# Optimization experiments

Hardware: AMD Instinct MI355X
Metric: run time of the kernel (lower is better)

The kernel has to match this reference:

```python
import jax, jax.numpy as jnp
import numpy as np

H = 1024  # hidden_size
NH = 16   # num_heads
HD = H // NH  # head_dim

def setup_inputs() -> dict:
    key = jax.random.key(0)
    ks = jax.random.split(key, 7)
    s = 1.0 / np.sqrt(H)
    return {
        "hidden": jax.random.normal(ks[0], (2, 2048, H), dtype=jnp.float32),
        "Wq": jax.random.normal(ks[1], (H, H), dtype=jnp.float32) * s,
        "bq": jnp.zeros((H,), dtype=jnp.float32),
        "Wk": jax.random.normal(ks[2], (H, H), dtype=jnp.float32) * s,
        "bk": jnp.zeros((H,), dtype=jnp.float32),
        "Wv": jax.random.normal(ks[3], (H, H), dtype=jnp.float32) * s,
        "bv": jnp.zeros((H,), dtype=jnp.float32),
    }

def _split_heads(x):
    # [B, S, H] -> [B, NH, S, HD]
    b, s, _ = x.shape
    return x.reshape(b, s, NH, HD).transpose(0, 2, 1, 3)

def reference(hidden, Wq, bq, Wk, bk, Wv, bv):
    q = _split_heads(hidden @ Wq.T + bq)
    k = _split_heads(hidden @ Wk.T + bk)
    v = _split_heads(hidden @ Wv.T + bv)
    scores = jnp.einsum("bhqd,bhkd->bhqk", q, k) / jnp.sqrt(jnp.float32(HD))
    probs = jax.nn.softmax(scores, axis=-1)  # dropout is identity in eval
    ctx = jnp.einsum("bhqk,bhkd->bhqd", probs, v)
    b, _, s, _ = ctx.shape
    return ctx.transpose(0, 2, 1, 3).reshape(b, s, NH * HD)
```

## Files before the change

### kernel.cpp

```cpp
#include <hip/hip_runtime.h>


typedef __attribute__((ext_vector_type(8))) short bf16x8;
typedef __attribute__((ext_vector_type(4))) short bf16x4;
typedef __attribute__((ext_vector_type(4))) float f32x4;

#define L2E 1.44269504088896340736f

__device__ __forceinline__ f32x4 mfma16(bf16x4 a, bf16x4 b, f32x4 c) {
#if defined(__AMDGCN__)
  return __builtin_amdgcn_mfma_f32_16x16x16bf16_1k(a, b, c, 0, 0, 0);
#else
  return c;
#endif
}

__device__ __forceinline__ unsigned short f2bf(float x) {
  union { float f; unsigned int u; } a; a.f = x;
  unsigned int r = (a.u + 0x7fffu + ((a.u >> 16) & 1u)) >> 16;
  return (unsigned short)r;
}
__device__ __forceinline__ unsigned int fbits(float x) {
  union { float f; unsigned int u; } a; a.f = x; return a.u;
}

__device__ __forceinline__ bf16x4 pack_bf16x4(float p0, float p1, float p2, float p3) {
#if defined(__AMDGCN__) && __has_builtin(__builtin_amdgcn_cvt_pk_bf16_f32)
  typedef __attribute__((ext_vector_type(2))) __bf16 bf16x2_t;
  union { bf16x2_t h[2]; bf16x4 v; } pk;
  pk.h[0] = __builtin_amdgcn_cvt_pk_bf16_f32(p0, p1);
  pk.h[1] = __builtin_amdgcn_cvt_pk_bf16_f32(p2, p3);
  return pk.v;
#else
  unsigned u0 = fbits(p0) + 0x8000u, u1 = fbits(p1) + 0x8000u;
  unsigned u2 = fbits(p2) + 0x8000u, u3 = fbits(p3) + 0x8000u;
  union { unsigned u[2]; bf16x4 v; } pk;
  pk.u[0] = __builtin_amdgcn_perm(u1, u0, 0x07060302u);
  pk.u[1] = __builtin_amdgcn_perm(u3, u2, 0x07060302u);
  return pk.v;
#endif
}

__device__ __forceinline__ void gl_lds16(const unsigned short* g, unsigned short* l) {
  __builtin_amdgcn_global_load_lds(
      (const __attribute__((address_space(1))) void*)g,
      (__attribute__((address_space(3))) void*)l, 16, 0, 0);
}

__global__ __launch_bounds__(256) void convert_all(
    const float* __restrict__ hidden, const float* __restrict__ Wq,
    const float* __restrict__ Wk, const float* __restrict__ Wv,
    unsigned short* __restrict__ Xb, unsigned short* __restrict__ Wqb,
    unsigned short* __restrict__ Wkb, unsigned short* __restrict__ Wvb) {
  int i = blockIdx.x * 256 + threadIdx.x;
  const float* src; unsigned short* dst; int off;
  if (i < 1048576)      { src = hidden; dst = Xb;  off = i; }
  else if (i < 1310720) { src = Wq;     dst = Wqb; off = i - 1048576; }
  else if (i < 1572864) { src = Wk;     dst = Wkb; off = i - 1310720; }
  else                  { src = Wv;     dst = Wvb; off = i - 1572864; }
  float4 v = ((const float4*)src)[off];
  ushort4 o;
  o.x = f2bf(v.x); o.y = f2bf(v.y); o.z = f2bf(v.z); o.w = f2bf(v.w);
  ((ushort4*)dst)[off] = o;
}

__global__ __launch_bounds__(256) void qkv_gemm(
    const unsigned short* __restrict__ Xb,
    const unsigned short* __restrict__ Wqb, const unsigned short* __restrict__ Wkb,
    const unsigned short* __restrict__ Wvb,
    const float* __restrict__ bq, const float* __restrict__ bk,
    const float* __restrict__ bv,
    unsigned short* __restrict__ Qh, unsigned short* __restrict__ Kh,
    unsigned short* __restrict__ Vh) {
  const int id  = blockIdx.x;
  const int xcd = id & 7;
  const int j   = id >> 3;
  const int tok = xcd * 4 + (j & 3);
  const int k2  = j >> 2;
  const int ft  = k2 & 7;
  const int z   = k2 >> 3;

  const unsigned short* Ap; const unsigned short* Bp;
  const float* bias; unsigned short* Out; int m0, n0;
  if (z == 2) {
    Ap = Wvb; Bp = Xb; bias = bv; Out = Vh;
    m0 = ft * 128; n0 = tok * 128;
  } else {
    Ap = Xb; Bp = (z == 0) ? Wqb : Wkb; bias = (z == 0) ? bq : bk;
    Out = (z == 0) ? Qh : Kh;
    m0 = tok * 128; n0 = ft * 128;
  }
  const float oscale = (z == 0) ? (0.125f * L2E) : 1.0f;

  __shared__ unsigned short As[128 * 64];
  __shared__ unsigned short Bs[128 * 64];

  const int tid  = threadIdx.x;
  const int lane = tid & 63;
  const int w    = tid >> 6;
  const int wm   = w >> 1, wn = w & 1;
  const int quad = lane >> 4;
  const int r    = lane & 15;

  f32x4 acc[4][4];
#pragma unroll
  for (int a = 0; a < 4; a++)
#pragma unroll
    for (int c = 0; c < 4; c++) acc[a][c] = (f32x4){0.f, 0.f, 0.f, 0.f};

  for (int k0 = 0; k0 < 1024; k0 += 64) {
    __syncthreads();
#pragma unroll
    for (int i = 0; i < 4; i++) {
      int t   = w * 4 + i;
      int blk = t * 64 + lane;
      int row = blk >> 3;
      int c   = (blk & 7) ^ (row & 7);
      gl_lds16(Ap + (size_t)(m0 + row) * 1024 + k0 + c * 8, &As[t * 512]);
      gl_lds16(Bp + (size_t)(n0 + row) * 1024 + k0 + c * 8, &Bs[t * 512]);
    }
    __syncthreads();

    bf16x8 af[4][2], bfv[4][2];
#pragma unroll
    for (int mi = 0; mi < 4; mi++)
#pragma unroll
      for (int ks = 0; ks < 2; ks++) {
        int row = wm * 64 + mi * 16 + r;
        int bc  = (ks * 4 + quad) ^ (row & 7);
        af[mi][ks] = *(const bf16x8*)&As[row * 64 + bc * 8];
      }
#pragma unroll
    for (int ni = 0; ni < 4; ni++)
#pragma unroll
      for (int ks = 0; ks < 2; ks++) {
        int row = wn * 64 + ni * 16 + r;
        int bc  = (ks * 4 + quad) ^ (row & 7);
        bfv[ni][ks] = *(const bf16x8*)&Bs[row * 64 + bc * 8];
      }
#pragma unroll
    for (int mi = 0; mi < 4; mi++)
#pragma unroll
      for (int ni = 0; ni < 4; ni++) {
        acc[mi][ni] = __builtin_amdgcn_mfma_f32_16x16x32_bf16(af[mi][0], bfv[ni][0], acc[mi][ni], 0, 0, 0);
        acc[mi][ni] = __builtin_amdgcn_mfma_f32_16x16x32_bf16(af[mi][1], bfv[ni][1], acc[mi][ni], 0, 0, 0);
      }
  }

  if (z == 2) {
#pragma unroll
    for (int mi = 0; mi < 4; mi++)
#pragma unroll
      for (int e = 0; e < 4; e++) {
        int m = m0 + wm * 64 + mi * 16 + quad * 4 + e;
        float bm = bias[m];
#pragma unroll
        for (int ni = 0; ni < 4; ni++) {
          int n = n0 + wn * 64 + ni * 16 + r;
          int bb = n >> 11, s = n & 2047;
          int hh = m >> 6,  d = m & 63;
          float v = acc[mi][ni][e] + bm;
          Out[((size_t)(bb * 16 + hh) * 64 + d) * 2048 + s] = f2bf(v);
        }
      }
  } else {
    float biasv[4];
#pragma unroll
    for (int ni = 0; ni < 4; ni++) biasv[ni] = bias[n0 + wn * 64 + ni * 16 + r];
#pragma unroll
    for (int mi = 0; mi < 4; mi++)
#pragma unroll
      for (int ni = 0; ni < 4; ni++)
#pragma unroll
        for (int e = 0; e < 4; e++) {
          int m = m0 + wm * 64 + mi * 16 + quad * 4 + e;
          int n = n0 + wn * 64 + ni * 16 + r;
          int bb = m >> 11, s = m & 2047;
          int hh = n >> 6,  d = n & 63;
          float v = (acc[mi][ni][e] + biasv[ni]) * oscale;
          Out[((size_t)(bb * 16 + hh) * 2048 + s) * 64 + d] = f2bf(v);
        }
  }
}

__global__ __launch_bounds__(256, 8) void attn(
    const unsigned short* __restrict__ Qh, const unsigned short* __restrict__ Kh,
    const unsigned short* __restrict__ Vh, float* __restrict__ accP,
    float* __restrict__ lP) {
  const int h = blockIdx.y;
  const int b = blockIdx.z >> 1;
  const int half = blockIdx.z & 1;
  const int bh = b * 16 + h;
  const int q0 = blockIdx.x * 64;
  const unsigned short* Qp  = Qh + (size_t)bh * 2048 * 64;
  const unsigned short* Kp  = Kh + (size_t)bh * 2048 * 64;
  const unsigned short* VTp = Vh + (size_t)bh * 64 * 2048;

  __shared__ unsigned short Ks[64 * 64];
  __shared__ unsigned short Vts[64 * 64];

  const int tid  = threadIdx.x;
  const int lane = tid & 63;
  const int w    = tid >> 6;
  const int quad = lane >> 4;
  const int r    = lane & 15;
  const int rm7  = r & 7;

  const unsigned short* qrow = Qp + (size_t)(q0 + w * 16 + r) * 64 + quad * 8;
  bf16x8 aq0 = *(const bf16x8*)(qrow);
  bf16x8 aq1 = *(const bf16x8*)(qrow + 32);

  float lsum = 0.f;
  f32x4 acc[4];
#pragma unroll
  for (int dc = 0; dc < 4; dc++) acc[dc] = (f32x4){0.f, 0.f, 0.f, 0.f};
  const f32x4 zero4 = (f32x4){0.f, 0.f, 0.f, 0.f};

  const int kx0 = quad ^ rm7;
  const int kx1 = (4 + quad) ^ rm7;
  const int qh2 = quad >> 1, ql4 = (quad & 1) * 4;

  const int kvbase = half * 1024;
  for (int kv0 = kvbase; kv0 < kvbase + 1024; kv0 += 64) {
    __syncthreads();
#pragma unroll
    for (int i = 0; i < 2; i++) {
      int blk = i * 256 + tid;
      int row = blk >> 3;
      int cs  = blk & 7;
      gl_lds16(Kp + (size_t)(kv0 + row) * 64 + ((cs ^ (row & 7)) * 8), &Ks[blk * 8]);
      gl_lds16(VTp + (size_t)row * 2048 + kv0 + (((cs + 5 * row) & 7) * 8), &Vts[blk * 8]);
    }
    __syncthreads();

#pragma unroll
    for (int nc = 0; nc < 4; nc++) {
      int krow = nc * 16 + r;
      bf16x8 kf0 = *(const bf16x8*)&Ks[krow * 64 + kx0 * 8];
      bf16x8 kf1 = *(const bf16x8*)&Ks[krow * 64 + kx1 * 8];

      f32x4 t0 = __builtin_amdgcn_mfma_f32_16x16x32_bf16(kf1, aq1, zero4, 0, 0, 0);
      f32x4 sT = __builtin_amdgcn_mfma_f32_16x16x32_bf16(kf0, aq0, t0, 0, 0, 0);

      float p0 = __builtin_exp2f(sT[0]);
      float p1 = __builtin_exp2f(sT[1]);
      float p2 = __builtin_exp2f(sT[2]);
      float p3 = __builtin_exp2f(sT[3]);
      lsum += (p0 + p1) + (p2 + p3);
      bf16x4 ap = pack_bf16x4(p0, p1, p2, p3);

#pragma unroll
      for (int dc = 0; dc < 4; dc++) {
        int vrow = dc * 16 + r;
        int slot = (2 * nc + qh2 + 3 * vrow) & 7;
        bf16x4 vf = *(const bf16x4*)&Vts[vrow * 64 + slot * 8 + ql4];
        acc[dc] = mfma16(ap, vf, acc[dc]);
      }
    }
  }

  lsum += __shfl_xor(lsum, 16, 64);
  lsum += __shfl_xor(lsum, 32, 64);
  if (lane < 16)
    lP[(size_t)half * 65536 + ((size_t)(b * 2048 + q0 + w * 16 + lane)) * 16 + h] = lsum;

  float* accp = accP + (size_t)half * 4194304;
#pragma unroll
  for (int e = 0; e < 4; e++) {
    int s = q0 + w * 16 + quad * 4 + e;
#pragma unroll
    for (int dc = 0; dc < 4; dc++) {
      int d = dc * 16 + r;
      accp[(size_t)(b * 2048 + s) * 1024 + h * 64 + d] = acc[dc][e];
    }
  }
}

__global__ __launch_bounds__(256) void merge_halves(
    const float* __restrict__ accP, const float* __restrict__ lP,
    float* __restrict__ out) {
  int i = blockIdx.x * 256 + threadIdx.x;
  int bs = i >> 8;
  int h  = (i & 255) >> 4;
  float l = lP[(size_t)bs * 16 + h] + lP[65536 + (size_t)bs * 16 + h];
  float inv = 1.f / l;
  float4 a0 = ((const float4*)accP)[i];
  float4 a1 = ((const float4*)accP)[1048576 + i];
  float4 o;
  o.x = (a0.x + a1.x) * inv;
  o.y = (a0.y + a1.y) * inv;
  o.z = (a0.z + a1.z) * inv;
  o.w = (a0.w + a1.w) * inv;
  ((float4*)out)[i] = o;
}

extern "C" void kernel_launch(void* const* d_in, const int* in_sizes, int n_in,
                              void* d_out, int out_size, void* d_ws, size_t ws_size,
                              hipStream_t stream) {
  const float* hidden = (const float*)d_in[0];
  const float* Wq = (const float*)d_in[1];
  const float* bq = (const float*)d_in[2];
  const float* Wk = (const float*)d_in[3];
  const float* bk = (const float*)d_in[4];
  const float* Wv = (const float*)d_in[5];
  const float* bv = (const float*)d_in[6];
  float* out = (float*)d_out;

  char* ws = (char*)d_ws;
  unsigned short* Qhp = (unsigned short*)(ws + 0);
  unsigned short* Khp = (unsigned short*)(ws + 8388608);
  unsigned short* Vhp = (unsigned short*)(ws + 16777216);
  unsigned short* Xb  = (unsigned short*)(ws + 25165824);
  unsigned short* Wqb = (unsigned short*)(ws + 33554432);
  unsigned short* Wkb = (unsigned short*)(ws + 35651584);
  unsigned short* Wvb = (unsigned short*)(ws + 37748736);
  float* accP = (float*)(ws + 25165824);
  float* lP   = (float*)(ws + 58720256);

  convert_all<<<7168, 256, 0, stream>>>(hidden, Wq, Wk, Wv, Xb, Wqb, Wkb, Wvb);
  qkv_gemm<<<768, 256, 0, stream>>>(Xb, Wqb, Wkb, Wvb, bq, bk, bv,
                                    Qhp, Khp, Vhp);
  attn<<<dim3(32, 16, 4), 256, 0, stream>>>(Qhp, Khp, Vhp, accP, lP);
  merge_halves<<<4096, 256, 0, stream>>>(accP, lP, out);
}
```

Before: 198.5 us.

## Merge KV-split halves inside attention block via LDS, drop merge kernel

The attention kernel now runs both KV halves in one 512-thread block, with each group of four waves owning a separate LDS K/V buffer. The halves are combined through shared memory and normalised in-kernel, removing the separate merge kernel and the fp32 partial-accumulator round trip through global memory. The row-sum is now computed with an MFMA against a ones vector instead of scalar adds and shuffles. The costs are larger blocks with doubled LDS per block, which may lower occupancy, and an extra block-wide sync at the end.

Result: faster. 184.0 us (-7.3%).

```diff
diff --git a/kernel.cpp b/kernel.cpp
--- a/kernel.cpp
+++ b/kernel.cpp
@@ -183,38 +183,44 @@
   }
 }
 
-__global__ __launch_bounds__(256, 8) void attn(
+__global__ __launch_bounds__(512, 8) void attn(
     const unsigned short* __restrict__ Qh, const unsigned short* __restrict__ Kh,
-    const unsigned short* __restrict__ Vh, float* __restrict__ accP,
-    float* __restrict__ lP) {
-  const int h = blockIdx.y;
-  const int b = blockIdx.z >> 1;
-  const int half = blockIdx.z & 1;
+    const unsigned short* __restrict__ Vh, float* __restrict__ Out) {
+  const int h = blockIdx.y, b = blockIdx.z;
   const int bh = b * 16 + h;
   const int q0 = blockIdx.x * 64;
   const unsigned short* Qp  = Qh + (size_t)bh * 2048 * 64;
   const unsigned short* Kp  = Kh + (size_t)bh * 2048 * 64;
   const unsigned short* VTp = Vh + (size_t)bh * 64 * 2048;
 
-  __shared__ unsigned short Ks[64 * 64];
-  __shared__ unsigned short Vts[64 * 64];
+  __shared__ unsigned short SM[2][2][64 * 64];
 
   const int tid  = threadIdx.x;
   const int lane = tid & 63;
-  const int w    = tid >> 6;
+  const int w8   = tid >> 6;
+  const int half = w8 >> 2;
+  const int w    = w8 & 3;
+  const int ltid = tid & 255;
   const int quad = lane >> 4;
   const int r    = lane & 15;
   const int rm7  = r & 7;
 
+  unsigned short* Ks  = &SM[half][0][0];
+  unsigned short* Vts = &SM[half][1][0];
+
   const unsigned short* qrow = Qp + (size_t)(q0 + w * 16 + r) * 64 + quad * 8;
   bf16x8 aq0 = *(const bf16x8*)(qrow);
   bf16x8 aq1 = *(const bf16x8*)(qrow + 32);
 
-  float lsum = 0.f;
+  f32x4 lacc = (f32x4){0.f, 0.f, 0.f, 0.f};
   f32x4 acc[4];
 #pragma unroll
   for (int dc = 0; dc < 4; dc++) acc[dc] = (f32x4){0.f, 0.f, 0.f, 0.f};
   const f32x4 zero4 = (f32x4){0.f, 0.f, 0.f, 0.f};
+
+  union { unsigned u[2]; bf16x4 v; } ou;
+  ou.u[0] = 0x3F803F80u; ou.u[1] = 0x3F803F80u;
+  const bf16x4 ones = ou.v;
 
   const int kx0 = quad ^ rm7;
   const int kx1 = (4 + quad) ^ rm7;
@@ -225,7 +231,7 @@
     __syncthreads();
 #pragma unroll
     for (int i = 0; i < 2; i++) {
-      int blk = i * 256 + tid;
+      int blk = i * 256 + ltid;
       int row = blk >> 3;
       int cs  = blk & 7;
       gl_lds16(Kp + (size_t)(kv0 + row) * 64 + ((cs ^ (row & 7)) * 8), &Ks[blk * 8]);
@@ -246,8 +252,9 @@
       float p1 = __builtin_exp2f(sT[1]);
       float p2 = __builtin_exp2f(sT[2]);
       float p3 = __builtin_exp2f(sT[3]);
-      lsum += (p0 + p1) + (p2 + p3);
       bf16x4 ap = pack_bf16x4(p0, p1, p2, p3);
+
+      lacc = mfma16(ap, ones, lacc);
 
 #pragma unroll
       for (int dc = 0; dc < 4; dc++) {
@@ -259,39 +266,35 @@
     }
   }
 
-  lsum += __shfl_xor(lsum, 16, 64);
-  lsum += __shfl_xor(lsum, 32, 64);
-  if (lane < 16)
-    lP[(size_t)half * 65536 + ((size_t)(b * 2048 + q0 + w * 16 + lane)) * 16 + h] = lsum;
-
-  float* accp = accP + (size_t)half * 4194304;
-#pragma unroll
-  for (int e = 0; e < 4; e++) {
-    int s = q0 + w * 16 + quad * 4 + e;
-#pragma unroll
-    for (int dc = 0; dc < 4; dc++) {
-      int d = dc * 16 + r;
-      accp[(size_t)(b * 2048 + s) * 1024 + h * 64 + d] = acc[dc][e];
-    }
-  }
-}
-
-__global__ __launch_bounds__(256) void merge_halves(
-    const float* __restrict__ accP, const float* __restrict__ lP,
-    float* __restrict__ out) {
-  int i = blockIdx.x * 256 + threadIdx.x;
-  int bs = i >> 8;
-  int h  = (i & 255) >> 4;
-  float l = lP[(size_t)bs * 16 + h] + lP[65536 + (size_t)bs * 16 + h];
-  float inv = 1.f / l;
-  float4 a0 = ((const float4*)accP)[i];
-  float4 a1 = ((const float4*)accP)[1048576 + i];
-  float4 o;
-  o.x = (a0.x + a1.x) * inv;
-  o.y = (a0.y + a1.y) * inv;
-  o.z = (a0.z + a1.z) * inv;
-  o.w = (a0.w + a1.w) * inv;
-  ((float4*)out)[i] = o;
+  __syncthreads();
+  float* Abuf = (float*)&SM[0][0][0];
+  float* Lbuf = Abuf + 64 * 65;
+  if (half == 1) {
+#pragma unroll
+    for (int e = 0; e < 4; e++) {
+      int q = w * 16 + quad * 4 + e;
+#pragma unroll
+      for (int dc = 0; dc < 4; dc++)
+        Abuf[q * 65 + dc * 16 + r] = acc[dc][e];
+      if (r == 0) Lbuf[q] = lacc[e];
+    }
+  }
+  __syncthreads();
+  if (half == 0) {
+#pragma unroll
+    for (int e = 0; e < 4; e++) {
+      int q = w * 16 + quad * 4 + e;
+      float l = lacc[e] + Lbuf[q];
+      float inv = 1.f / l;
+      int s = q0 + q;
+#pragma unroll
+      for (int dc = 0; dc < 4; dc++) {
+        int d = dc * 16 + r;
+        float v = acc[dc][e] + Abuf[q * 65 + d];
+        Out[(size_t)(b * 2048 + s) * 1024 + h * 64 + d] = v * inv;
+      }
+    }
+  }
 }
 
 extern "C" void kernel_launch(void* const* d_in, const int* in_sizes, int n_in,
@@ -314,12 +317,9 @@
   unsigned short* Wqb = (unsigned short*)(ws + 33554432);
   unsigned short* Wkb = (unsigned short*)(ws + 35651584);
   unsigned short* Wvb = (unsigned short*)(ws + 37748736);
-  float* accP = (float*)(ws + 25165824);
-  float* lP   = (float*)(ws + 58720256);
 
   convert_all<<<7168, 256, 0, stream>>>(hidden, Wq, Wk, Wv, Xb, Wqb, Wkb, Wvb);
   qkv_gemm<<<768, 256, 0, stream>>>(Xb, Wqb, Wkb, Wvb, bq, bk, bv,
                                     Qhp, Khp, Vhp);
-  attn<<<dim3(32, 16, 4), 256, 0, stream>>>(Qhp, Khp, Vhp, accP, lP);
-  merge_halves<<<4096, 256, 0, stream>>>(accP, lP, out);
-}
+  attn<<<dim3(32, 16, 2), 512, 0, stream>>>(Qhp, Khp, Vhp, out);
+}
```
